# Performance work log

Measured on AMD Instinct MI355X. Metric: run time of the kernel, lower is better.

The kernel has to match this reference:

```python
import jax, jax.numpy as jnp
import numpy as np

HEADS = 16
KV_HEADS = 8
DIMS = 64
IN_DIMS = 1024
B, S = 2, 2048


def rope(x):
    # RoPE applied over the FULL flattened last dim (heads*dims), as in the source.
    seq_len, dim = x.shape[-2], x.shape[-1]
    thetas = 1.0 / 10000 ** (jnp.arange(0, dim, 2) / dim)          # [dim/2]
    ang = jnp.arange(1, seq_len + 1)[:, None] * thetas[None, :]    # [S, dim/2] (positions start at 1)
    cos, sin = jnp.cos(ang), jnp.sin(ang)
    xe, xo = x[..., ::2], x[..., 1::2]
    real = xe * cos - xo * sin
    imag = xe * sin + xo * cos
    return jnp.stack([real, imag], axis=-1).reshape(x.shape)


def setup_inputs() -> dict:
    key = jax.random.key(0)
    k1, k2, k3, k4, k5 = jax.random.split(key, 5)
    q = jax.random.normal(k1, (B, S, IN_DIMS), dtype=jnp.float32)
    sd = 1.0 / np.sqrt(IN_DIMS)
    Wq = jax.random.normal(k2, (IN_DIMS, HEADS * DIMS), dtype=jnp.float32) * sd
    Wk = jax.random.normal(k3, (IN_DIMS, KV_HEADS * DIMS), dtype=jnp.float32) * sd
    Wv = jax.random.normal(k4, (IN_DIMS, KV_HEADS * DIMS), dtype=jnp.float32) * sd
    Wo = jax.random.normal(k5, (HEADS * DIMS, IN_DIMS), dtype=jnp.float32) / np.sqrt(HEADS * DIMS)
    return {"q": q, "Wq": Wq, "Wk": Wk, "Wv": Wv, "Wo": Wo}


def reference(q, Wq, Wk, Wv, Wo):
    batch, seq_len, in_dims = q.shape
    kv = q  # self-attention (kv=None path)
    xq = rope(q @ Wq)            # [B, S, H*D], RoPE over flattened dim
    xk = rope(kv @ Wk)           # [B, S, Hk*D]
    xv = kv @ Wv                 # [B, S, Hk*D]
    # element-wise repeat(2) on last axis, exactly as source (interleaved duplication)
    xk = jnp.repeat(xk, 2, axis=-1)   # [B, S, H*D]
    xv = jnp.repeat(xv, 2, axis=-1)
    xq = xq.reshape(batch, seq_len, HEADS, DIMS).transpose(0, 2, 1, 3)  # [B,H,S,D]
    xk = xk.reshape(batch, seq_len, HEADS, DIMS).transpose(0, 2, 3, 1)  # [B,H,D,S]
    xv = xv.reshape(batch, seq_len, HEADS, DIMS).transpose(0, 2, 1, 3)  # [B,H,S,D]
    scale = (DIMS / HEADS) ** (-0.5)  # source uses dims/heads, not 1/sqrt(dims)
    scores = jax.nn.softmax((xq @ xk) * scale, axis=-1)  # [B,H,S,S]
    out = (scores @ xv).transpose(0, 2, 1, 3).reshape(batch, seq_len, -1)
    return out @ Wo
```

## Files before the change

kernel.cpp:

```cpp
#include <hip/hip_runtime.h>
#include <hip/hip_bf16.h>
#include <math.h>

#define HEADS 16
#define KV_HEADS 8
#define DIMS 64
#define IN_DIMS 1024
#define BATCH 2
#define SEQ 2048

typedef __attribute__((ext_vector_type(8))) short short8;
typedef __attribute__((ext_vector_type(4))) float f32x4;
typedef __attribute__((ext_vector_type(4))) unsigned int u32x4;

__device__ __forceinline__ short f2bf(float f) {
    __hip_bfloat16 h = __float2bfloat16(f);
    return *reinterpret_cast<short*>(&h);
}

__device__ __forceinline__ float e2(float x) {
    return __builtin_amdgcn_exp2f(x);
}

__device__ __forceinline__ unsigned int cvtpk(float a, float b) {
    unsigned int r;
    asm("v_cvt_pk_bf16_f32 %0, %1, %2" : "=v"(r) : "v"(a), "v"(b));
    return r;
}

__device__ __forceinline__ void gl_lds16(const void* g, void* l) {
    __builtin_amdgcn_global_load_lds(
        (const __attribute__((address_space(1))) unsigned int*)g,
        (__attribute__((address_space(3))) unsigned int*)l, 16, 0, 0);
}

#define LOG2_10000 13.287712379549449f
#define LOG2_2PI   2.6514961294723187f
#define CSCALE (0.5f * 1.4426950408889634f)

__device__ __forceinline__ void sincos_rev(float ang_rev, float* sn, float* cs) {
    float fr = ang_rev - floorf(ang_rev);
    *sn = __builtin_amdgcn_sinf(fr);
    *cs = __builtin_amdgcn_cosf(fr);
}

__global__ __launch_bounds__(256) void prep_weights(
    const float* __restrict__ Wq, const float* __restrict__ Wk,
    const float* __restrict__ Wv, const float* __restrict__ Wo,
    short* __restrict__ WT, short* __restrict__ WoPt,
    const float* __restrict__ qin, short* __restrict__ Abf)
{
    __shared__ float t[32][33];
    int z = blockIdx.z;
    if (z >= 4) {
        int i = (z - 4) * 1024 + blockIdx.y * 32 + blockIdx.x;
        size_t idx = ((size_t)i * 256 + threadIdx.x) * 8;
        float4 a = *(const float4*)(qin + idx);
        float4 c = *(const float4*)(qin + idx + 4);
        u32x4 s = { cvtpk(a.x, a.y), cvtpk(a.z, a.w),
                    cvtpk(c.x, c.y), cvtpk(c.z, c.w) };
        *(u32x4*)(Abf + idx) = s;
        return;
    }
    int bx = blockIdx.x * 32, by = blockIdx.y * 32;
    int x = threadIdx.x & 31, y = threadIdx.x >> 5;
    if (z == 3) {
        if (by >= 512) return;
        #pragma unroll
        for (int i = 0; i < 32; i += 8) {
            int d = by + y + i;
            t[y + i][x] = Wo[(size_t)(2 * d) * 1024 + bx + x]
                        + Wo[(size_t)(2 * d + 1) * 1024 + bx + x];
        }
        __syncthreads();
        #pragma unroll
        for (int i = 0; i < 32; i += 8)
            WoPt[(size_t)(bx + y + i) * 512 + by + x] = f2bf(t[x][y + i]);
    } else {
        const float* W = (z == 0) ? Wq : ((z == 1) ? Wk : Wv);
        int N = (z == 0) ? 1024 : 512;
        if (bx >= N) return;
        short* dst = WT + ((z == 0) ? 0 : ((z == 1) ? (size_t)1024 * 1024
                                                    : (size_t)1536 * 1024));
        #pragma unroll
        for (int i = 0; i < 32; i += 8)
            t[y + i][x] = W[(size_t)(by + y + i) * N + bx + x];
        __syncthreads();
        #pragma unroll
        for (int i = 0; i < 32; i += 8)
            dst[(size_t)(bx + y + i) * 1024 + by + x] = f2bf(t[x][y + i]);
    }
}

__global__ __launch_bounds__(256) void gemm_af32(
    const short* __restrict__ A, const short* __restrict__ Bt,
    float* __restrict__ C, int M, int N, int K)
{
    __shared__ short As[128][64];
    __shared__ short Bs[128][64];

    int tid  = threadIdx.x;
    int lane = tid & 63, wave = tid >> 6;
    int quad = lane >> 4, ln = lane & 15;
    int wm = (wave >> 1) * 64, wn = (wave & 1) * 64;
    int row0 = blockIdx.y * 128, col0 = blockIdx.x * 128;

    int sr = lane >> 3;
    int sk = (lane & 7) * 8;

    f32x4 acc[4][4] = {};

    for (int kt = 0; kt < K; kt += 64) {
        #pragma unroll
        for (int u = 0; u < 4; ++u) {
            int r = wave * 32 + u * 8;
            gl_lds16(A + (size_t)(row0 + r + sr) * K + kt + sk, &As[r][0]);
        }
        #pragma unroll
        for (int u = 0; u < 4; ++u) {
            int r = wave * 32 + u * 8;
            gl_lds16(Bt + (size_t)(col0 + r + sr) * K + kt + sk, &Bs[r][0]);
        }
        __syncthreads();

        #pragma unroll
        for (int k0 = 0; k0 < 64; k0 += 32) {
            short8 af[4], bfr[4];
            #pragma unroll
            for (int i = 0; i < 4; ++i)
                af[i] = *(const short8*)&As[wm + 16 * i + ln][k0 + quad * 8];
            #pragma unroll
            for (int j = 0; j < 4; ++j)
                bfr[j] = *(const short8*)&Bs[wn + 16 * j + ln][k0 + quad * 8];
            #pragma unroll
            for (int i = 0; i < 4; ++i)
                #pragma unroll
                for (int j = 0; j < 4; ++j)
                    acc[i][j] = __builtin_amdgcn_mfma_f32_16x16x32_bf16(
                        af[i], bfr[j], acc[i][j], 0, 0, 0);
        }
        __syncthreads();
    }

    #pragma unroll
    for (int i = 0; i < 4; ++i)
        #pragma unroll
        for (int j = 0; j < 4; ++j)
            #pragma unroll
            for (int r = 0; r < 4; ++r)
                C[(size_t)(row0 + wm + 16 * i + quad * 4 + r) * N
                  + col0 + wn + 16 * j + ln] = acc[i][j][r];
}

__global__ __launch_bounds__(256) void prep_qkv(
    const float* __restrict__ XQKV, short* __restrict__ Qp,
    short* __restrict__ Kb, short* __restrict__ Vtg)
{
    __shared__ float t[32][33];
    int blk = blockIdx.x;
    if (blk < 8192) {
        int idx = blk * 256 + threadIdx.x;
        int row = idx >> 9;
        int i   = idx & 511;
        int pos = row & (SEQ - 1);
        float tr = e2(-2.f * (float)i / 1024.f * LOG2_10000 - LOG2_2PI);
        float sn, cs;
        sincos_rev((float)(pos + 1) * tr, &sn, &cs);
        float2 x = *(const float2*)(XQKV + (size_t)row * 2048 + 2 * i);
        Qp[(size_t)row * 512 + i] = f2bf((x.x * (cs + sn) + x.y * (cs - sn)) * CSCALE);
    } else if (blk < 12288) {
        int idx = (blk - 8192) * 256 + threadIdx.x;
        int row = idx >> 8;
        int i   = idx & 255;
        int pos = row & (SEQ - 1);
        float tr = e2(-2.f * (float)i / 512.f * LOG2_10000 - LOG2_2PI);
        float sn, cs;
        sincos_rev((float)(pos + 1) * tr, &sn, &cs);
        float2 x = *(const float2*)(XQKV + (size_t)row * 2048 + 1024 + 2 * i);
        unsigned int o = cvtpk(x.x * cs - x.y * sn, x.x * sn + x.y * cs);
        *(unsigned int*)(Kb + (size_t)row * 512 + 2 * i) = o;
    } else {
        int id = blk - 12288;
        int bx = (id & 15) * 32;
        int by = ((id >> 4) & 63) * 32;
        int b  = id >> 10;
        int x = threadIdx.x & 31, y = threadIdx.x >> 5;
        #pragma unroll
        for (int i = 0; i < 32; i += 8)
            t[y + i][x] = XQKV[(size_t)(b * SEQ + by + y + i) * 2048 + 1536 + bx + x];
        __syncthreads();
        #pragma unroll
        for (int i = 0; i < 32; i += 8)
            Vtg[((size_t)b * 512 + bx + y + i) * SEQ + by + x] = f2bf(t[x][y + i]);
    }
}

__global__ __launch_bounds__(512) void flash_attn(
    const short* __restrict__ Qp, const short* __restrict__ Kb,
    const short* __restrict__ Vtg, short* __restrict__ AO32)
{
    __shared__ short Qs[128][40];
    __shared__ short Ks[2][64][40];
    __shared__ short Vt[2][32][72];

    int tid = threadIdx.x;
    int qt = blockIdx.x & 15;
    int h  = (blockIdx.x >> 4) & 15;
    int b  = blockIdx.x >> 8;

    int lane = tid & 63, wave = tid >> 6;
    int quad = lane >> 4, ln = lane & 15;
    int qw = wave * 16;

    {
        int row = tid >> 2, off = (tid & 3) * 8;
        *(short8*)&Qs[row][off] =
            *(const short8*)(Qp + (size_t)(b * SEQ + qt * 128 + row) * 512 + h * 32 + off);
    }

    const short* Kgb = Kb + (size_t)(b * SEQ) * 512 + 32 * h;
    const short* Vgb = Vtg + ((size_t)b * 512 + 32 * h) * SEQ;

    bool doK = tid < 256;
    int st = tid & 255;
    int krow = st >> 2, koff = (st & 3) * 8;
    int prow = ((krow >> 5) << 5) | (((krow >> 2) & 1) << 4)
             | (((krow >> 3) & 3) << 2) | (krow & 3);
    int vrow = st >> 3, voff = (st & 7) * 8;

    short8 sreg;
    if (doK) {
        sreg = *(const short8*)(Kgb + (size_t)krow * 512 + koff);
        *(short8*)&Ks[0][prow][koff] = sreg;
    } else {
        sreg = *(const short8*)(Vgb + (size_t)vrow * SEQ + voff);
        *(short8*)&Vt[0][vrow][voff] = sreg;
    }
    __syncthreads();

    short8 af = *(const short8*)&Qs[qw + ln][quad * 8];

    float lsum = 0.f;
    f32x4 Oacc[2] = {};
    const f32x4 zz = {};

    for (int t = 0; t < 32; ++t) {
        int cur = t & 1;

        if (t < 31) {
            int ktn = (t + 1) * 64;
            if (doK)
                sreg = *(const short8*)(Kgb + (size_t)(ktn + krow) * 512 + koff);
            else
                sreg = *(const short8*)(Vgb + (size_t)vrow * SEQ + ktn + voff);
        }

        f32x4 sc[4];
        __builtin_amdgcn_s_setprio(1);
        #pragma unroll
        for (int j0 = 0; j0 < 4; ++j0) {
            short8 kf = *(const short8*)&Ks[cur][j0 * 16 + ln][quad * 8];
            sc[j0] = __builtin_amdgcn_mfma_f32_16x16x32_bf16(kf, af, zz, 0, 0, 0);
        }
        __builtin_amdgcn_s_setprio(0);

        short8 pf[2];
        #pragma unroll
        for (int kg = 0; kg < 2; ++kg) {
            float p0 = e2(sc[2 * kg][0]);
            float p1 = e2(sc[2 * kg][1]);
            float p2 = e2(sc[2 * kg][2]);
            float p3 = e2(sc[2 * kg][3]);
            float p4 = e2(sc[2 * kg + 1][0]);
            float p5 = e2(sc[2 * kg + 1][1]);
            float p6 = e2(sc[2 * kg + 1][2]);
            float p7 = e2(sc[2 * kg + 1][3]);
            lsum += ((p0 + p1) + (p2 + p3)) + ((p4 + p5) + (p6 + p7));
            short8 s = { f2bf(p0), f2bf(p1), f2bf(p2), f2bf(p3),
                         f2bf(p4), f2bf(p5), f2bf(p6), f2bf(p7) };
            pf[kg] = s;
        }

        __builtin_amdgcn_s_setprio(1);
        #pragma unroll
        for (int kg = 0; kg < 2; ++kg) {
            #pragma unroll
            for (int ng = 0; ng < 2; ++ng) {
                short8 vf = *(const short8*)&Vt[cur][ng * 16 + ln][kg * 32 + quad * 8];
                Oacc[ng] = __builtin_amdgcn_mfma_f32_16x16x32_bf16(
                    vf, pf[kg], Oacc[ng], 0, 0, 0);
            }
        }
        __builtin_amdgcn_s_setprio(0);

        if (t < 31) {
            if (doK) *(short8*)&Ks[cur ^ 1][prow][koff] = sreg;
            else     *(short8*)&Vt[cur ^ 1][vrow][voff] = sreg;
        }
        __syncthreads();
    }

    lsum += __shfl_xor(lsum, 16);
    lsum += __shfl_xor(lsum, 32);
    float inv = 1.f / lsum;

    size_t row = (size_t)(b * SEQ) + qt * 128 + qw + ln;
    #pragma unroll
    for (int ng = 0; ng < 2; ++ng) {
        short4 o4 = { f2bf(Oacc[ng][0] * inv), f2bf(Oacc[ng][1] * inv),
                      f2bf(Oacc[ng][2] * inv), f2bf(Oacc[ng][3] * inv) };
        *(short4*)&AO32[row * 512 + h * 32 + ng * 16 + quad * 4] = o4;
    }
}

__global__ __launch_bounds__(256) void gemm_wo(
    const short* __restrict__ A, const short* __restrict__ Bt,
    float* __restrict__ C)
{
    __shared__ short As[64][64];
    __shared__ short Bs[128][64];

    int tid  = threadIdx.x;
    int lane = tid & 63, wave = tid >> 6;
    int quad = lane >> 4, ln = lane & 15;
    int wm = (wave >> 1) * 32, wn = (wave & 1) * 64;
    int row0 = blockIdx.y * 64, col0 = blockIdx.x * 128;
    const int K = 512, N = 1024;

    int sr = lane >> 3;
    int sk = (lane & 7) * 8;

    f32x4 acc[2][4] = {};

    for (int kt = 0; kt < K; kt += 64) {
        #pragma unroll
        for (int u = 0; u < 2; ++u) {
            int r = wave * 16 + u * 8;
            gl_lds16(A + (size_t)(row0 + r + sr) * K + kt + sk, &As[r][0]);
        }
        #pragma unroll
        for (int u = 0; u < 4; ++u) {
            int r = wave * 32 + u * 8;
            gl_lds16(Bt + (size_t)(col0 + r + sr) * K + kt + sk, &Bs[r][0]);
        }
        __syncthreads();

        #pragma unroll
        for (int k0 = 0; k0 < 64; k0 += 32) {
            short8 af[2], bfr[4];
            #pragma unroll
            for (int i = 0; i < 2; ++i)
                af[i] = *(const short8*)&As[wm + 16 * i + ln][k0 + quad * 8];
            #pragma unroll
            for (int j = 0; j < 4; ++j)
                bfr[j] = *(const short8*)&Bs[wn + 16 * j + ln][k0 + quad * 8];
            #pragma unroll
            for (int i = 0; i < 2; ++i)
                #pragma unroll
                for (int j = 0; j < 4; ++j)
                    acc[i][j] = __builtin_amdgcn_mfma_f32_16x16x32_bf16(
                        af[i], bfr[j], acc[i][j], 0, 0, 0);
        }
        __syncthreads();
    }

    #pragma unroll
    for (int i = 0; i < 2; ++i)
        #pragma unroll
        for (int j = 0; j < 4; ++j)
            #pragma unroll
            for (int r = 0; r < 4; ++r)
                C[(size_t)(row0 + wm + 16 * i + quad * 4 + r) * N
                  + col0 + wn + 16 * j + ln] = acc[i][j][r];
}

extern "C" void kernel_launch(void* const* d_in, const int* in_sizes, int n_in,
                              void* d_out, int out_size, void* d_ws, size_t ws_size,
                              hipStream_t stream)
{
    const float* q  = (const float*)d_in[0];
    const float* Wq = (const float*)d_in[1];
    const float* Wk = (const float*)d_in[2];
    const float* Wv = (const float*)d_in[3];
    const float* Wo = (const float*)d_in[4];
    float* out = (float*)d_out;

    const int M = BATCH * SEQ;

    float* XQKV = (float*)d_ws;
    short* WT   = (short*)(XQKV + (size_t)M * 2048);
    short* WoPt = WT + (size_t)2048 * 1024;
    short* Qp   = WoPt + (size_t)1024 * 512;
    short* Kb   = Qp + (size_t)M * 512;
    short* Vtg  = Kb + (size_t)M * 512;
    short* AO32 = WT;
    short* Abf  = Qp;

    dim3 blk(256);

    prep_weights<<<dim3(32, 32, 6), blk, 0, stream>>>(Wq, Wk, Wv, Wo, WT, WoPt, q, Abf);

    gemm_af32<<<dim3(16, 32), blk, 0, stream>>>(Abf, WT, XQKV, M, 2048, 1024);

    prep_qkv<<<14336, blk, 0, stream>>>(XQKV, Qp, Kb, Vtg);

    flash_attn<<<BATCH * HEADS * (SEQ / 128), dim3(512), 0, stream>>>(Qp, Kb, Vtg, AO32);

    gemm_wo<<<dim3(8, 64), blk, 0, stream>>>(AO32, WoPt, out);
}
```

Measured before the change: 157.9 us.

## Fuse RoPE, bf16 conversion and V transpose into QKV GEMM epilogue

The QKV projection GEMM now applies RoPE to the Q and K columns in its epilogue, using lane shuffles to pair even and odd elements, and writes bf16 Qp/Kb directly. V columns are written transposed into Vtg. This removes the fp32 XQKV intermediate round trip through global memory and the separate prep_qkv launch. In exchange, the epilogue does more sincos work per element and issues strided, half-masked stores, and the workspace layout moves Abf into the old XQKV region.

```diff
diff --git a/kernel.cpp b/kernel.cpp
--- a/kernel.cpp
+++ b/kernel.cpp
@@ -92,10 +92,11 @@
     }
 }
 
-__global__ __launch_bounds__(256) void gemm_af32(
+__global__ __launch_bounds__(256) void gemm_qkv(
     const short* __restrict__ A, const short* __restrict__ Bt,
-    float* __restrict__ C, int M, int N, int K)
+    short* __restrict__ Qp, short* __restrict__ Kb, short* __restrict__ Vtg)
 {
+    const int K = 1024;
     __shared__ short As[128][64];
     __shared__ short Bs[128][64];
 
@@ -142,56 +143,60 @@
         __syncthreads();
     }
 
-    #pragma unroll
-    for (int i = 0; i < 4; ++i)
-        #pragma unroll
-        for (int j = 0; j < 4; ++j)
-            #pragma unroll
-            for (int r = 0; r < 4; ++r)
-                C[(size_t)(row0 + wm + 16 * i + quad * 4 + r) * N
-                  + col0 + wn + 16 * j + ln] = acc[i][j][r];
-}
-
-__global__ __launch_bounds__(256) void prep_qkv(
-    const float* __restrict__ XQKV, short* __restrict__ Qp,
-    short* __restrict__ Kb, short* __restrict__ Vtg)
-{
-    __shared__ float t[32][33];
-    int blk = blockIdx.x;
-    if (blk < 8192) {
-        int idx = blk * 256 + threadIdx.x;
-        int row = idx >> 9;
-        int i   = idx & 511;
-        int pos = row & (SEQ - 1);
-        float tr = e2(-2.f * (float)i / 1024.f * LOG2_10000 - LOG2_2PI);
-        float sn, cs;
-        sincos_rev((float)(pos + 1) * tr, &sn, &cs);
-        float2 x = *(const float2*)(XQKV + (size_t)row * 2048 + 2 * i);
-        Qp[(size_t)row * 512 + i] = f2bf((x.x * (cs + sn) + x.y * (cs - sn)) * CSCALE);
-    } else if (blk < 12288) {
-        int idx = (blk - 8192) * 256 + threadIdx.x;
-        int row = idx >> 8;
-        int i   = idx & 255;
-        int pos = row & (SEQ - 1);
-        float tr = e2(-2.f * (float)i / 512.f * LOG2_10000 - LOG2_2PI);
-        float sn, cs;
-        sincos_rev((float)(pos + 1) * tr, &sn, &cs);
-        float2 x = *(const float2*)(XQKV + (size_t)row * 2048 + 1024 + 2 * i);
-        unsigned int o = cvtpk(x.x * cs - x.y * sn, x.x * sn + x.y * cs);
-        *(unsigned int*)(Kb + (size_t)row * 512 + 2 * i) = o;
+    bool evn = (lane & 1) == 0;
+
+    if (col0 < 1024) {
+        #pragma unroll
+        for (int j = 0; j < 4; ++j) {
+            int col = col0 + wn + 16 * j + ln;
+            float tr = e2(-(float)(col & ~1) / 1024.f * LOG2_10000 - LOG2_2PI);
+            #pragma unroll
+            for (int i = 0; i < 4; ++i)
+                #pragma unroll
+                for (int r = 0; r < 4; ++r) {
+                    int row = row0 + wm + 16 * i + quad * 4 + r;
+                    float xe = acc[i][j][r];
+                    float xo = __shfl_xor(xe, 1);
+                    float sn, cs;
+                    sincos_rev((float)((row & (SEQ - 1)) + 1) * tr, &sn, &cs);
+                    float o = (xe * (cs + sn) + xo * (cs - sn)) * CSCALE;
+                    if (evn)
+                        Qp[(size_t)row * 512 + (col >> 1)] = f2bf(o);
+                }
+        }
+    } else if (col0 < 1536) {
+        #pragma unroll
+        for (int j = 0; j < 4; ++j) {
+            int c = col0 + wn + 16 * j + ln - 1024;
+            float tr = e2(-(float)(c & ~1) / 512.f * LOG2_10000 - LOG2_2PI);
+            #pragma unroll
+            for (int i = 0; i < 4; ++i)
+                #pragma unroll
+                for (int r = 0; r < 4; ++r) {
+                    int row = row0 + wm + 16 * i + quad * 4 + r;
+                    float xe = acc[i][j][r];
+                    float xo = __shfl_xor(xe, 1);
+                    float sn, cs;
+                    sincos_rev((float)((row & (SEQ - 1)) + 1) * tr, &sn, &cs);
+                    unsigned int o = cvtpk(xe * cs - xo * sn, xe * sn + xo * cs);
+                    if (evn)
+                        *(unsigned int*)(Kb + (size_t)row * 512 + c) = o;
+                }
+        }
     } else {
-        int id = blk - 12288;
-        int bx = (id & 15) * 32;
-        int by = ((id >> 4) & 63) * 32;
-        int b  = id >> 10;
-        int x = threadIdx.x & 31, y = threadIdx.x >> 5;
-        #pragma unroll
-        for (int i = 0; i < 32; i += 8)
-            t[y + i][x] = XQKV[(size_t)(b * SEQ + by + y + i) * 2048 + 1536 + bx + x];
-        __syncthreads();
-        #pragma unroll
-        for (int i = 0; i < 32; i += 8)
-            Vtg[((size_t)b * 512 + bx + y + i) * SEQ + by + x] = f2bf(t[x][y + i]);
+        int b = row0 >> 11;
+        int s0 = (row0 & (SEQ - 1)) + wm + quad * 4;
+        #pragma unroll
+        for (int j = 0; j < 4; ++j) {
+            int dim = col0 + wn + 16 * j + ln - 1536;
+            short* dst = Vtg + ((size_t)(b * 512 + dim)) * SEQ + s0;
+            #pragma unroll
+            for (int i = 0; i < 4; ++i) {
+                short4 o4 = { f2bf(acc[i][j][0]), f2bf(acc[i][j][1]),
+                              f2bf(acc[i][j][2]), f2bf(acc[i][j][3]) };
+                *(short4*)(dst + 16 * i) = o4;
+            }
+        }
     }
 }
 
@@ -387,22 +392,19 @@
 
     const int M = BATCH * SEQ;
 
-    float* XQKV = (float*)d_ws;
-    short* WT   = (short*)(XQKV + (size_t)M * 2048);
+    short* Abf  = (short*)d_ws;
+    short* WT   = (short*)((float*)d_ws + (size_t)M * 2048);
     short* WoPt = WT + (size_t)2048 * 1024;
     short* Qp   = WoPt + (size_t)1024 * 512;
     short* Kb   = Qp + (size_t)M * 512;
     short* Vtg  = Kb + (size_t)M * 512;
     short* AO32 = WT;
-    short* Abf  = Qp;
 
     dim3 blk(256);
 
     prep_weights<<<dim3(32, 32, 6), blk, 0, stream>>>(Wq, Wk, Wv, Wo, WT, WoPt, q, Abf);
 
-    gemm_af32<<<dim3(16, 32), blk, 0, stream>>>(Abf, WT, XQKV, M, 2048, 1024);
-
-    prep_qkv<<<14336, blk, 0, stream>>>(XQKV, Qp, Kb, Vtg);
+    gemm_qkv<<<dim3(16, 32), blk, 0, stream>>>(Abf, WT, Qp, Kb, Vtg);
 
     flash_attn<<<BATCH * HEADS * (SEQ / 128), dim3(512), 0, stream>>>(Qp, Kb, Vtg, AO32);
 
```

Result: slower. 171.7 us (+8.8%).
